# Kernel optimization log

Measured on AMD Instinct MI355X. Metric: run time of the kernel, lower is better.

Reference implementation:

```python
import jax, jax.numpy as jnp
import numpy as np
import math

B, T, C, H = 8, 1024, 1024, 16
D = C // H  # head_size = 64
FF = 4 * C


def setup_inputs() -> dict:
    key = jax.random.key(0)
    ks = jax.random.split(key, 8)
    s = 0.02
    return {
        "x": jax.random.normal(ks[0], (B, T, C), jnp.float32),
        "ln1_g": jnp.ones((C,), jnp.float32),
        "ln1_b": jnp.zeros((C,), jnp.float32),
        "attn_w": jax.random.normal(ks[1], (C, 3 * C), jnp.float32) * s,
        "attn_b": jnp.zeros((3 * C,), jnp.float32),
        "attn_proj_w": jax.random.normal(ks[2], (C, C), jnp.float32) * s,
        "attn_proj_b": jnp.zeros((C,), jnp.float32),
        "ln2_g": jnp.ones((C,), jnp.float32),
        "ln2_b": jnp.zeros((C,), jnp.float32),
        "fc_w": jax.random.normal(ks[3], (C, FF), jnp.float32) * s,
        "fc_b": jnp.zeros((FF,), jnp.float32),
        "mlp_proj_w": jax.random.normal(ks[4], (FF, C), jnp.float32) * s,
        "mlp_proj_b": jnp.zeros((C,), jnp.float32),
    }


def _layernorm(x, g, b, eps=1e-5):
    mu = jnp.mean(x, axis=-1, keepdims=True)
    var = jnp.mean(jnp.square(x - mu), axis=-1, keepdims=True)
    return (x - mu) * jax.lax.rsqrt(var + eps) * g + b


def reference(x, ln1_g, ln1_b, attn_w, attn_b, attn_proj_w, attn_proj_b,
              ln2_g, ln2_b, fc_w, fc_b, mlp_proj_w, mlp_proj_b):
    # --- attention branch (pre-LN) ---
    h = _layernorm(x, ln1_g, ln1_b)
    kqv = h @ attn_w + attn_b                      # (B,T,3C)
    # NOTE: source splits as k, q, v (k first!)
    k, q, v = jnp.split(kqv, 3, axis=-1)
    k = k.reshape(B, T, H, D).transpose(0, 2, 1, 3)  # (B,H,T,D)
    q = q.reshape(B, T, H, D).transpose(0, 2, 1, 3)
    v = v.reshape(B, T, H, D).transpose(0, 2, 1, 3)
    # NOTE: source computes k @ q^T, i.e. wei[i,j] = k_i . q_j
    scale = 1.0 / math.sqrt(D)
    wei = jnp.einsum('bhid,bhjd->bhij', k, q) * scale  # (B,H,T,T)
    causal = jnp.tril(jnp.ones((T, T), dtype=bool))
    wei = jnp.where(causal, wei, -jnp.inf)
    wei = jax.nn.softmax(wei, axis=-1)
    out = jnp.einsum('bhij,bhjd->bhid', wei, v)        # (B,H,T,D)
    out = out.transpose(0, 2, 1, 3).reshape(B, T, C)
    out = out @ attn_proj_w + attn_proj_b
    x = x + out
    # --- MLP branch (pre-LN) ---
    h2 = _layernorm(x, ln2_g, ln2_b)
    m = jax.nn.gelu(h2 @ fc_w + fc_b, approximate=False)  # torch GELU default = exact erf
    m = m @ mlp_proj_w + mlp_proj_b
    return x + m
```

## Files before the change

### kernel.cpp

```cpp
#include <hip/hip_runtime.h>
#include <stdint.h>

typedef unsigned short u16;
typedef __bf16 bf16x8 __attribute__((ext_vector_type(8)));
typedef float f32x4 __attribute__((ext_vector_type(4)));

#define DEVINL static __device__ __forceinline__

DEVINL u16 f2bf(float f) {
  uint32_t u = __builtin_bit_cast(uint32_t, f);
  u += 0x7fffu + ((u >> 16) & 1u);
  return (u16)(u >> 16);
}

DEVINL uint32_t pack_bf2(float f0, float f1) {
  uint32_t u0 = __builtin_bit_cast(uint32_t, f0) + 0x8000u;
  uint32_t u1 = __builtin_bit_cast(uint32_t, f1) + 0x8000u;
  return __builtin_amdgcn_perm(u1, u0, 0x07060302u);
}

DEVINL bf16x8 ld_frag(const u16* p) { return *(const bf16x8*)p; }

DEVINL void gld_lds16(const void* g, void* l) {
  __builtin_amdgcn_global_load_lds((const __attribute__((address_space(1))) void*)g,
                                   (__attribute__((address_space(3))) void*)l, 16, 0, 0);
}

DEVINL void xcd_tile_wide(int& tm, int& tn) {
  const int gx = gridDim.x;
  const int flat = blockIdx.x + gx * blockIdx.y;
  const int q = (gx * gridDim.y) >> 3;
  const int wg = (flat & 7) * q + (flat >> 3);
  tn = (wg % gx) * 128;
  tm = (wg / gx) * 256;
}

__global__ __launch_bounds__(256)
void transpose_bf16(const float* __restrict__ W, u16* __restrict__ Wt, int K, int N) {
  __shared__ float tile[32][33];
  const int n0 = blockIdx.x * 32, k0 = blockIdx.y * 32;
  const int tx = threadIdx.x, ty = threadIdx.y;
#pragma unroll
  for (int i = 0; i < 32; i += 8)
    tile[ty + i][tx] = W[(size_t)(k0 + ty + i) * N + n0 + tx];
  __syncthreads();
#pragma unroll
  for (int i = 0; i < 32; i += 8)
    Wt[(size_t)(n0 + ty + i) * K + k0 + tx] = f2bf(tile[tx][ty + i]);
}

__global__ __launch_bounds__(256)
void ln_kernel(const float* __restrict__ x, const float* __restrict__ g,
               const float* __restrict__ b, u16* __restrict__ out) {
  __shared__ float red[8];
  const size_t row = blockIdx.x;
  const int tid = threadIdx.x;
  float4 v = ((const float4*)(x + row * 1024))[tid];
  float s = v.x + v.y + v.z + v.w;
  float s2 = v.x * v.x + v.y * v.y + v.z * v.z + v.w * v.w;
#pragma unroll
  for (int o = 32; o; o >>= 1) { s += __shfl_down(s, o); s2 += __shfl_down(s2, o); }
  const int w = tid >> 6;
  if ((tid & 63) == 0) { red[w * 2] = s; red[w * 2 + 1] = s2; }
  __syncthreads();
  const float S = red[0] + red[2] + red[4] + red[6];
  const float S2 = red[1] + red[3] + red[5] + red[7];
  const float mu = S * (1.f / 1024.f);
  const float var = S2 * (1.f / 1024.f) - mu * mu;
  const float rstd = rsqrtf(var + 1e-5f);
  float4 gv = ((const float4*)g)[tid];
  float4 bv = ((const float4*)b)[tid];
  ushort4 o;
  o.x = f2bf((v.x - mu) * rstd * gv.x + bv.x);
  o.y = f2bf((v.y - mu) * rstd * gv.y + bv.y);
  o.z = f2bf((v.z - mu) * rstd * gv.z + bv.z);
  o.w = f2bf((v.w - mu) * rstd * gv.w + bv.w);
  ((ushort4*)(out + row * 1024))[tid] = o;
}

enum { EPI_KQV = 0, EPI_RESID = 1, EPI_GELU = 2, EPI_ADD = 3 };

template <int EPI>
DEVINL void gemm_epilogue(f32x4 (&acc)[4][4], const float* __restrict__ bias,
                          void* __restrict__ outp, const float* __restrict__ resid,
                          int N, int tm, int tn, int mh, int nh, int q4, int c) {
#pragma unroll
  for (int mt = 0; mt < 4; ++mt) {
#pragma unroll
    for (int nt = 0; nt < 4; ++nt) {
      const int col = tn + nh + nt * 16 + c;
      const float bcol = bias[col];
#pragma unroll
      for (int rg = 0; rg < 4; ++rg) {
        const int row = tm + mh + mt * 16 + q4 * 4 + rg;
        float val = acc[mt][nt][rg] + bcol;
        if constexpr (EPI == EPI_KQV) {
          const int bb = row >> 10, t = row & 1023;
          const int s = col >> 10, rem = col & 1023;
          const int hh = rem >> 6, d = rem & 63;
          if (s == 0) val *= 0.18033688011112042f;
          const size_t base = ((size_t)((bb * 16 + hh) * 3 + s)) << 16;
          const size_t idx = (s == 2) ? base + (size_t)d * 1024 + t : base + (size_t)t * 64 + d;
          ((u16*)outp)[idx] = f2bf(val);
        } else if constexpr (EPI == EPI_RESID) {
          const size_t idx = (size_t)row * 1024 + col;
          ((float*)outp)[idx] = val + resid[idx];
        } else if constexpr (EPI == EPI_GELU) {
          const float x2 = val * val;
          const float t = __builtin_fmaf(x2, -0.102952445f, -2.30221235f);
          const float e = __builtin_amdgcn_exp2f(val * t);
          const float ge = val * __builtin_amdgcn_rcpf(1.0f + e);
          ((u16*)outp)[(size_t)row * N + col] = f2bf(ge);
        } else {
          const size_t idx = (size_t)row * 1024 + col;
          ((float*)outp)[idx] += val;
        }
      }
    }
  }
}

template <int EPI>
DEVINL void gemm_bodyW(const u16* __restrict__ A, const u16* __restrict__ Bt,
                       const float* __restrict__ bias, void* __restrict__ outp,
                       const float* __restrict__ resid, int N, int K,
                       int tm, int tn) {
  __shared__ alignas(16) u16 sT[3][48 * 512];
  const int tid = threadIdx.x;
  const int w = tid >> 6, l = tid & 63;
  const int q4 = l >> 4, c = l & 15;
  const int mh = (w >> 1) * 64, nh = (w & 1) * 64;

  f32x4 acc[4][4] = {};

  const int lr = l >> 3;
  const int lc = ((l & 7) ^ lr) * 8;
  const u16* gA[4];
  const u16* gB[2];
#pragma unroll
  for (int j = 0; j < 4; ++j) gA[j] = A + (size_t)(tm + 32 * w + j * 8 + lr) * K + lc;
#pragma unroll
  for (int j = 0; j < 2; ++j) gB[j] = Bt + (size_t)(tn + 16 * w + j * 8 + lr) * K + lc;

  auto stageW = [&](int buf, int k0) {
#pragma unroll
    for (int j = 0; j < 4; ++j) gld_lds16(gA[j] + k0, &sT[buf][(4 * w + j) * 512]);
#pragma unroll
    for (int j = 0; j < 2; ++j) gld_lds16(gB[j] + k0, &sT[buf][(32 + 2 * w + j) * 512]);
  };

  auto computeW = [&](int cur) {
    const u16* bufA = sT[cur];
    const u16* bufB = sT[cur] + 32 * 512;
#pragma unroll
    for (int kh = 0; kh < 2; ++kh) {
      bf16x8 af[4], bfv[4];
#pragma unroll
      for (int mt = 0; mt < 4; ++mt) {
        const int row = mh + mt * 16 + c;
        af[mt] = ld_frag(bufA + row * 64 + ((kh * 4 + q4) ^ (c & 7)) * 8);
      }
#pragma unroll
      for (int nt = 0; nt < 4; ++nt) {
        const int row = nh + nt * 16 + c;
        bfv[nt] = ld_frag(bufB + row * 64 + ((kh * 4 + q4) ^ (c & 7)) * 8);
      }
      __builtin_amdgcn_s_setprio(1);
#pragma unroll
      for (int mt = 0; mt < 4; ++mt)
#pragma unroll
        for (int nt = 0; nt < 4; ++nt)
          acc[mt][nt] = __builtin_amdgcn_mfma_f32_16x16x32_bf16(af[mt], bfv[nt], acc[mt][nt], 0, 0, 0);
      __builtin_amdgcn_s_setprio(0);
    }
  };

  const int nI = K / 64;
  stageW(0, 0);
  stageW(1, 64);
  int bc = 0;
  int i = 0;
  for (; i < nI - 1; ++i) {
    asm volatile("s_waitcnt vmcnt(6)" ::: "memory");
    __builtin_amdgcn_s_barrier();
    asm volatile("" ::: "memory");
    if (i + 2 < nI) {
      const int tgt = (bc >= 1) ? bc - 1 : 2;
      stageW(tgt, (i + 2) * 64);
    }
    computeW(bc);
    bc = (bc < 2) ? bc + 1 : 0;
  }
  asm volatile("s_waitcnt vmcnt(0)" ::: "memory");
  __builtin_amdgcn_s_barrier();
  asm volatile("" ::: "memory");
  computeW(bc);

  gemm_epilogue<EPI>(acc, bias, outp, resid, N, tm, tn, mh, nh, q4, c);
}

__global__ __launch_bounds__(512)
void gemm_kqv(const u16* __restrict__ A, const u16* __restrict__ Bt,
              const float* __restrict__ bias, u16* __restrict__ outp,
              int M, int N, int K) {
  int tm, tn;
  xcd_tile_wide(tm, tn);
  gemm_bodyW<EPI_KQV>(A, Bt, bias, outp, nullptr, N, K, tm, tn);
}

__global__ __launch_bounds__(512)
void gemm_gelu(const u16* __restrict__ A, const u16* __restrict__ Bt,
               const float* __restrict__ bias, u16* __restrict__ outp,
               int M, int N, int K) {
  int tm, tn;
  xcd_tile_wide(tm, tn);
  gemm_bodyW<EPI_GELU>(A, Bt, bias, outp, nullptr, N, K, tm, tn);
}

__global__ __launch_bounds__(512)
void gemm_resid(const u16* __restrict__ A, const u16* __restrict__ Bt,
                const float* __restrict__ bias, float* __restrict__ outp,
                const float* __restrict__ resid, int M, int N, int K) {
  int tm, tn;
  xcd_tile_wide(tm, tn);
  gemm_bodyW<EPI_RESID>(A, Bt, bias, outp, resid, N, K, tm, tn);
}

__global__ __launch_bounds__(512)
void gemm_add(const u16* __restrict__ A, const u16* __restrict__ Bt,
              const float* __restrict__ bias, float* __restrict__ outp,
              int M, int N, int K) {
  int tm, tn;
  xcd_tile_wide(tm, tn);
  gemm_bodyW<EPI_ADD>(A, Bt, bias, outp, nullptr, N, K, tm, tn);
}

__global__ __launch_bounds__(256)
void attn_kernel(const u16* __restrict__ kqv, u16* __restrict__ outp) {
  constexpr int LS = 72;
  __shared__ alignas(16) u16 sP[64 * LS];
  __shared__ alignas(16) u16 sK[64 * LS];
  __shared__ alignas(16) u16 sV[64 * LS];
  const int bh = blockIdx.x;
  const int it = (int)gridDim.y - 1 - (int)blockIdx.y;
  const int tid = threadIdx.x;
  const int w = tid >> 6, l = tid & 63, q4 = l >> 4, c = l & 15;
  const int il = w * 16 + c;
  const size_t hb = (size_t)bh * 3 * 65536;
  const u16* qbase = kqv + hb;
  const u16* kbase = kqv + hb + 65536;
  const u16* vbase = kqv + hb + 2 * 65536;

  const int sr = tid >> 3, sc = (tid & 7) * 8;
  const int sr2 = sr + 32;
  *(int4*)&sP[sr * LS + sc] = *(const int4*)(qbase + (size_t)(it * 64 + sr) * 64 + sc);
  *(int4*)&sP[sr2 * LS + sc] = *(const int4*)(qbase + (size_t)(it * 64 + sr2) * 64 + sc);

  f32x4 oacc[4] = {};
  float lsum = 0.f;
  bf16x8 bq0, bq1;

  for (int jt = 0; jt <= it; ++jt) {
    if (jt) __syncthreads();
    *(int4*)&sK[sr * LS + sc] = *(const int4*)(kbase + (size_t)(jt * 64 + sr) * 64 + sc);
    *(int4*)&sK[sr2 * LS + sc] = *(const int4*)(kbase + (size_t)(jt * 64 + sr2) * 64 + sc);
    *(int4*)&sV[sr * LS + sc] = *(const int4*)(vbase + (size_t)sr * 1024 + jt * 64 + sc);
    *(int4*)&sV[sr2 * LS + sc] = *(const int4*)(vbase + (size_t)sr2 * 1024 + jt * 64 + sc);
    __syncthreads();
    if (jt == 0) {
      bq0 = ld_frag(sP + il * LS + q4 * 8);
      bq1 = ld_frag(sP + il * LS + 32 + q4 * 8);
    }

    f32x4 st[4] = {};
#pragma unroll
    for (int nt = 0; nt < 4; ++nt) {
      st[nt] = __builtin_amdgcn_mfma_f32_16x16x32_bf16(
          ld_frag(sK + (nt * 16 + c) * LS + q4 * 8), bq0, st[nt], 0, 0, 0);
      st[nt] = __builtin_amdgcn_mfma_f32_16x16x32_bf16(
          ld_frag(sK + (nt * 16 + c) * LS + 32 + q4 * 8), bq1, st[nt], 0, 0, 0);
    }

    const bool diag = (jt == it);
    u16* prow = sP + il * LS;
#pragma unroll
    for (int nt = 0; nt < 4; ++nt) {
      float e0 = __builtin_amdgcn_exp2f(st[nt][0]);
      float e1 = __builtin_amdgcn_exp2f(st[nt][1]);
      float e2 = __builtin_amdgcn_exp2f(st[nt][2]);
      float e3 = __builtin_amdgcn_exp2f(st[nt][3]);
      if (diag) {
        const int jb = nt * 16 + q4 * 4;
        e0 = (jb + 0 > il) ? 0.f : e0;
        e1 = (jb + 1 > il) ? 0.f : e1;
        e2 = (jb + 2 > il) ? 0.f : e2;
        e3 = (jb + 3 > il) ? 0.f : e3;
      }
      lsum += (e0 + e1) + (e2 + e3);
      uint2 pk = {pack_bf2(e0, e1), pack_bf2(e2, e3)};
      *(uint2*)&prow[nt * 16 + q4 * 4] = pk;
    }

    bf16x8 bp0 = ld_frag(sP + il * LS + q4 * 8);
    bf16x8 bp1 = ld_frag(sP + il * LS + 32 + q4 * 8);
#pragma unroll
    for (int dt = 0; dt < 4; ++dt) {
      oacc[dt] = __builtin_amdgcn_mfma_f32_16x16x32_bf16(
          ld_frag(sV + (dt * 16 + c) * LS + q4 * 8), bp0, oacc[dt], 0, 0, 0);
      oacc[dt] = __builtin_amdgcn_mfma_f32_16x16x32_bf16(
          ld_frag(sV + (dt * 16 + c) * LS + 32 + q4 * 8), bp1, oacc[dt], 0, 0, 0);
    }
  }

  lsum += __shfl_xor(lsum, 16);
  lsum += __shfl_xor(lsum, 32);
  const float linv = 1.f / lsum;

  const int b_ = bh >> 4, h_ = bh & 15;
  const int t_ = it * 64 + il;
  u16* orow = outp + ((size_t)(b_ * 1024 + t_)) * 1024 + h_ * 64;
#pragma unroll
  for (int dt = 0; dt < 4; ++dt) {
    uint2 ok = {pack_bf2(oacc[dt][0] * linv, oacc[dt][1] * linv),
                pack_bf2(oacc[dt][2] * linv, oacc[dt][3] * linv)};
    *(uint2*)&orow[dt * 16 + q4 * 4] = ok;
  }
}

extern "C" void kernel_launch(void* const* d_in, const int* in_sizes, int n_in,
                              void* d_out, int out_size, void* d_ws, size_t ws_size,
                              hipStream_t stream) {
  const float* x       = (const float*)d_in[0];
  const float* ln1_g   = (const float*)d_in[1];
  const float* ln1_b   = (const float*)d_in[2];
  const float* attn_w  = (const float*)d_in[3];
  const float* attn_b  = (const float*)d_in[4];
  const float* attn_pw = (const float*)d_in[5];
  const float* attn_pb = (const float*)d_in[6];
  const float* ln2_g   = (const float*)d_in[7];
  const float* ln2_b   = (const float*)d_in[8];
  const float* fc_w    = (const float*)d_in[9];
  const float* fc_b    = (const float*)d_in[10];
  const float* mlp_w   = (const float*)d_in[11];
  const float* mlp_b   = (const float*)d_in[12];
  float* out = (float*)d_out;

  u16* ws = (u16*)d_ws;
  u16* mlpT     = ws;
  u16* attn_wT  = mlpT + 1024 * 4096;
  u16* attn_pwT = attn_wT + 3072 * 1024;
  u16* fcT      = attn_pwT + 1024 * 1024;
  u16* hbuf     = fcT + 4096 * 1024;
  u16* kqv      = hbuf + 8192 * 1024;
  u16* attn_o   = kqv + (size_t)8192 * 3072;
  u16* mbuf     = kqv;

  dim3 tb(32, 8);
  transpose_bf16<<<dim3(96, 32),  tb, 0, stream>>>(attn_w,  attn_wT,  1024, 3072);
  transpose_bf16<<<dim3(32, 32),  tb, 0, stream>>>(attn_pw, attn_pwT, 1024, 1024);
  transpose_bf16<<<dim3(128, 32), tb, 0, stream>>>(fc_w,    fcT,      1024, 4096);
  transpose_bf16<<<dim3(32, 128), tb, 0, stream>>>(mlp_w,   mlpT,     4096, 1024);

  ln_kernel<<<8192, 256, 0, stream>>>(x, ln1_g, ln1_b, hbuf);

  gemm_kqv<<<dim3(24, 32), 512, 0, stream>>>(hbuf, attn_wT, attn_b, kqv, 8192, 3072, 1024);

  attn_kernel<<<dim3(128, 16), 256, 0, stream>>>(kqv, attn_o);

  gemm_resid<<<dim3(8, 32), 512, 0, stream>>>(attn_o, attn_pwT, attn_pb, out, x,
                                              8192, 1024, 1024);

  ln_kernel<<<8192, 256, 0, stream>>>(out, ln2_g, ln2_b, hbuf);

  gemm_gelu<<<dim3(32, 32), 512, 0, stream>>>(hbuf, fcT, fc_b, mbuf, 8192, 4096, 1024);

  gemm_add<<<dim3(8, 32), 512, 0, stream>>>(mbuf, mlpT, mlp_b, out, 8192, 1024, 4096);
}
```

Measured before the change: 463.8 us.

## Split GEMM k-step into two halves interleaving LDS reads, global staging and MFMAs

Restructures the triple-buffered wide GEMM main loop so each 64-wide k step is split into two 32-wide halves. Each half issues its LDS fragment reads and half of the next-next tile's global-to-LDS loads, then synchronises and runs 16 MFMAs, with barriers placed to keep waves in lockstep. The intent is a ping-pong style schedule that overlaps memory issue with matrix math more finely. It adds four barriers per iteration, which may cost more than the overlap gains.

```diff
diff --git a/kernel.cpp b/kernel.cpp
--- a/kernel.cpp
+++ b/kernel.cpp
@@ -142,59 +142,66 @@
 #pragma unroll
   for (int j = 0; j < 2; ++j) gB[j] = Bt + (size_t)(tn + 16 * w + j * 8 + lr) * K + lc;
 
-  auto stageW = [&](int buf, int k0) {
-#pragma unroll
-    for (int j = 0; j < 4; ++j) gld_lds16(gA[j] + k0, &sT[buf][(4 * w + j) * 512]);
-#pragma unroll
-    for (int j = 0; j < 2; ++j) gld_lds16(gB[j] + k0, &sT[buf][(32 + 2 * w + j) * 512]);
+  auto stageHalfA = [&](int buf, int k0) {
+    gld_lds16(gA[0] + k0, &sT[buf][(4 * w + 0) * 512]);
+    gld_lds16(gA[1] + k0, &sT[buf][(4 * w + 1) * 512]);
+    gld_lds16(gB[0] + k0, &sT[buf][(32 + 2 * w + 0) * 512]);
   };
-
-  auto computeW = [&](int cur) {
+  auto stageHalfB = [&](int buf, int k0) {
+    gld_lds16(gA[2] + k0, &sT[buf][(4 * w + 2) * 512]);
+    gld_lds16(gA[3] + k0, &sT[buf][(4 * w + 3) * 512]);
+    gld_lds16(gB[1] + k0, &sT[buf][(32 + 2 * w + 1) * 512]);
+  };
+  auto stageFull = [&](int buf, int k0) { stageHalfA(buf, k0); stageHalfB(buf, k0); };
+
+  auto readFrags = [&](int cur, int kh, bf16x8 (&af)[4], bf16x8 (&bf)[4]) {
     const u16* bufA = sT[cur];
     const u16* bufB = sT[cur] + 32 * 512;
-#pragma unroll
-    for (int kh = 0; kh < 2; ++kh) {
-      bf16x8 af[4], bfv[4];
-#pragma unroll
-      for (int mt = 0; mt < 4; ++mt) {
-        const int row = mh + mt * 16 + c;
-        af[mt] = ld_frag(bufA + row * 64 + ((kh * 4 + q4) ^ (c & 7)) * 8);
-      }
-#pragma unroll
-      for (int nt = 0; nt < 4; ++nt) {
-        const int row = nh + nt * 16 + c;
-        bfv[nt] = ld_frag(bufB + row * 64 + ((kh * 4 + q4) ^ (c & 7)) * 8);
-      }
-      __builtin_amdgcn_s_setprio(1);
-#pragma unroll
-      for (int mt = 0; mt < 4; ++mt)
-#pragma unroll
-        for (int nt = 0; nt < 4; ++nt)
-          acc[mt][nt] = __builtin_amdgcn_mfma_f32_16x16x32_bf16(af[mt], bfv[nt], acc[mt][nt], 0, 0, 0);
-      __builtin_amdgcn_s_setprio(0);
-    }
+    const int ko = ((kh * 4 + q4) ^ (c & 7)) * 8;
+#pragma unroll
+    for (int mt = 0; mt < 4; ++mt) af[mt] = ld_frag(bufA + (mh + mt * 16 + c) * 64 + ko);
+#pragma unroll
+    for (int nt = 0; nt < 4; ++nt) bf[nt] = ld_frag(bufB + (nh + nt * 16 + c) * 64 + ko);
   };
+  auto mfma16 = [&](bf16x8 (&af)[4], bf16x8 (&bf)[4]) {
+    __builtin_amdgcn_s_setprio(1);
+#pragma unroll
+    for (int mt = 0; mt < 4; ++mt)
+#pragma unroll
+      for (int nt = 0; nt < 4; ++nt)
+        acc[mt][nt] = __builtin_amdgcn_mfma_f32_16x16x32_bf16(af[mt], bf[nt], acc[mt][nt], 0, 0, 0);
+    __builtin_amdgcn_s_setprio(0);
+  };
 
   const int nI = K / 64;
-  stageW(0, 0);
-  stageW(1, 64);
+  stageFull(0, 0);
+  stageFull(1, 64);
+  asm volatile("s_waitcnt vmcnt(6)" ::: "memory");
+  __builtin_amdgcn_s_barrier();
+
   int bc = 0;
-  int i = 0;
-  for (; i < nI - 1; ++i) {
-    asm volatile("s_waitcnt vmcnt(6)" ::: "memory");
+  for (int i = 0; i < nI; ++i) {
+    const int tgt = (bc >= 1) ? bc - 1 : 2;
+    const bool st = (i + 2 < nI);
+    bf16x8 af[4], bf[4];
+    readFrags(bc, 0, af, bf);
+    if (st) stageHalfA(tgt, (i + 2) * 64);
     __builtin_amdgcn_s_barrier();
-    asm volatile("" ::: "memory");
-    if (i + 2 < nI) {
-      const int tgt = (bc >= 1) ? bc - 1 : 2;
-      stageW(tgt, (i + 2) * 64);
-    }
-    computeW(bc);
+    asm volatile("s_waitcnt lgkmcnt(0)" ::: "memory");
+    mfma16(af, bf);
+    __builtin_amdgcn_s_barrier();
+    readFrags(bc, 1, af, bf);
+    if (st) stageHalfB(tgt, (i + 2) * 64);
+    if (i + 1 < nI) {
+      if (st) asm volatile("s_waitcnt vmcnt(6)" ::: "memory");
+      else    asm volatile("s_waitcnt vmcnt(0)" ::: "memory");
+    }
+    __builtin_amdgcn_s_barrier();
+    asm volatile("s_waitcnt lgkmcnt(0)" ::: "memory");
+    mfma16(af, bf);
+    __builtin_amdgcn_s_barrier();
     bc = (bc < 2) ? bc + 1 : 0;
   }
-  asm volatile("s_waitcnt vmcnt(0)" ::: "memory");
-  __builtin_amdgcn_s_barrier();
-  asm volatile("" ::: "memory");
-  computeW(bc);
 
   gemm_epilogue<EPI>(acc, bias, outp, resid, N, tm, tn, mh, nh, q4, c);
 }
```

Measured after the change: 466.9 us. About the same (+0.7%).
